# Optimization experiments

Measured on AMD Instinct MI355X. Metric: run time of the kernel, lower is better.

Reference implementation:

```python
import jax, jax.numpy as jnp
import numpy as np

B, T, D = 8, 2048, 256  # batch, time segments, feature dim (a_dim=v_dim=hidden=out=256)
EPS = 1e-8


def _layer_norm(x, g, b, eps=1e-6):
    m = jnp.mean(x, axis=-1, keepdims=True)
    v = jnp.var(x, axis=-1, keepdims=True)
    return (x - m) * jax.lax.rsqrt(v + eps) * g + b


def setup_inputs() -> dict:
    key = jax.random.key(0)
    ks = jax.random.split(key, 9)
    xav = lambda k: jax.random.uniform(k, (D, D), jnp.float32, -1.0, 1.0) * np.sqrt(6.0 / (D + D))
    return {
        "a_fea": jax.random.normal(ks[0], (B, T, D), jnp.float32),
        "v_fea": jax.random.normal(ks[1], (B, T, D), jnp.float32),
        "thr_val": jnp.float32(0.099),
        "Wv1": xav(ks[2]), "Wv2": xav(ks[3]), "Wvfc": xav(ks[4]),
        "Wa1": xav(ks[5]), "Wa2": xav(ks[6]), "Wafc": xav(ks[7]),
        "ln_g": jnp.ones((D,), jnp.float32),
        "ln_b": jnp.zeros((D,), jnp.float32),
    }


def reference(a_fea, v_fea, thr_val, Wv1, Wv2, Wvfc, Wa1, Wa2, Wafc, ln_g, ln_b):
    relu = jax.nn.relu
    # branch projections (dropout is identity at eval); torch Linear: x @ W.T
    v1 = relu(jnp.einsum('btd,hd->bth', v_fea, Wv1))
    v2 = relu(jnp.einsum('btd,hd->bth', v_fea, Wv2))
    a1 = relu(jnp.einsum('btd,hd->bth', a_fea, Wa1))
    a2 = relu(jnp.einsum('btd,hd->bth', a_fea, Wa2))

    d = v2.shape[-1]
    # scaled cross-modal scores, ReLU'd  [B, Tv, Ta]
    beta_va = relu(jnp.einsum('btd,bsd->bts', v2, a1) / jnp.sqrt(jnp.float32(d)))
    # a->v scores taken BEFORE row-normalization of beta_va (as in torch code)
    beta_av = jnp.transpose(beta_va, (0, 2, 1))

    time = beta_va.shape[-1]
    thr = thr_val * 10.0 / time

    # normalize -> threshold sparsify -> renormalize (v attends to a)
    bn_va = beta_va / (jnp.sum(beta_va, axis=-1, keepdims=True) + EPS)
    g_va = jnp.where(bn_va > thr, bn_va, 0.0)
    g_va = g_va / (jnp.sum(g_va, axis=-1, keepdims=True) + EPS)

    # same for a attends to v
    bn_av = beta_av / (jnp.sum(beta_av, axis=-1, keepdims=True) + EPS)
    g_av = jnp.where(bn_av > thr, bn_av, 0.0)
    g_av = g_av / (jnp.sum(g_av, axis=-1, keepdims=True) + EPS)

    # vectorized form of the diagonal selection double-loop (batch element 0)
    pred = (jnp.diagonal(g_av[0]) > 0).astype(jnp.float32)  # [T]

    a_pos = jnp.einsum('bts,bsd->btd', g_va, a2)
    v_psp = v_fea + a_pos
    v_pos = jnp.einsum('bts,bsd->btd', g_av, v1)
    a_psp = a_fea + v_pos

    v_psp = _layer_norm(relu(jnp.einsum('btd,od->bto', v_psp, Wvfc)), ln_g, ln_b)
    a_psp = _layer_norm(relu(jnp.einsum('btd,od->bto', a_psp, Wafc)), ln_g, ln_b)
    a_v_fuse = 0.5 * (v_psp + a_psp)
    return a_v_fuse, v_psp, a_psp, pred
```

## Files before the change

kernel.cpp:

```cpp
#include <hip/hip_runtime.h>
#include <math.h>

#define TT 2048
#define DD 256
#define NBATCH 8
#define EPSF 1e-8f

typedef unsigned short u16;
typedef __attribute__((ext_vector_type(8))) short short8;
typedef __attribute__((ext_vector_type(4))) float f32x4;

__device__ __forceinline__ u16 f2bf(float x) {
    unsigned int u = __builtin_bit_cast(unsigned int, x);
    u += 0x7fffu + ((u >> 16) & 1u);
    return (u16)(u >> 16);
}
__device__ __forceinline__ float bf2f(u16 h) {
    return __builtin_bit_cast(float, (unsigned int)h << 16);
}

__device__ __forceinline__ int frag_dst(int row, int k) {
    return (((row >> 4) * 4 + (k >> 3)) * 16 + (row & 15)) * 8 + (k & 7);
}

template<int BR>
__device__ __forceinline__ void stage_tile(const u16* __restrict__ g, u16* s,
                                           int row0, int k0, int ldk, int tid)
{
    #pragma unroll
    for (int i = 0; i < BR / 64; ++i) {
        const int c = tid + 256 * i;
        const int row = c >> 2, q = c & 3;
        *(int4*)(s + frag_dst(row, q * 8)) =
            *(const int4*)(g + (long)(row0 + row) * ldk + k0 + q * 8);
    }
}

__global__ __launch_bounds__(256)
void proj_kernel(const u16* __restrict__ vfh, const u16* __restrict__ vfl,
                 const u16* __restrict__ afh, const u16* __restrict__ afl,
                 const u16* __restrict__ Wsp,
                 u16* __restrict__ v2h, u16* __restrict__ v2l,
                 u16* __restrict__ a1h, u16* __restrict__ a1l,
                 u16* __restrict__ v1T, u16* __restrict__ a2T)
{
    const int zz = blockIdx.z;
    const u16* Ah = (zz == 1 || zz == 3) ? afh : vfh;
    const u16* Al = (zz == 1 || zz == 3) ? afl : vfl;
    const int widx = (zz == 0) ? 2 : (zz == 1) ? 4 : (zz == 2) ? 0 : 6;
    const u16* Bh = Wsp + widx * DD * DD;
    const u16* Bl = Bh + DD * DD;
    const bool split = zz < 2;
    u16* Oh = (zz == 0) ? v2h : a1h;
    u16* Ol = (zz == 0) ? v2l : a1l;
    u16* OT = (zz == 2) ? v1T : a2T;

    __shared__ __align__(16) u16 Ah_s[64 * 32], Al_s[64 * 32];
    __shared__ __align__(16) u16 Bh_s[64 * 32], Bl_s[64 * 32];
    const int m0 = blockIdx.y * 64, n0 = blockIdx.x * 64;
    const int tid = threadIdx.x, lane = tid & 63, w = tid >> 6;
    const int wy = w >> 1, wx = w & 1;
    f32x4 acc[2][2] = {};

    for (int k0 = 0; k0 < DD; k0 += 32) {
        stage_tile<64>(Ah, Ah_s, m0, k0, DD, tid);
        stage_tile<64>(Al, Al_s, m0, k0, DD, tid);
        stage_tile<64>(Bh, Bh_s, n0, k0, DD, tid);
        stage_tile<64>(Bl, Bl_s, n0, k0, DD, tid);
        __syncthreads();
        short8 ah[2], al[2], bh[2], bl[2];
        #pragma unroll
        for (int i = 0; i < 2; ++i) {
            ah[i] = *(const short8*)(Ah_s + ((wy * 2 + i) * 64 + lane) * 8);
            al[i] = *(const short8*)(Al_s + ((wy * 2 + i) * 64 + lane) * 8);
        }
        #pragma unroll
        for (int j = 0; j < 2; ++j) {
            bh[j] = *(const short8*)(Bh_s + ((wx * 2 + j) * 64 + lane) * 8);
            bl[j] = *(const short8*)(Bl_s + ((wx * 2 + j) * 64 + lane) * 8);
        }
        #pragma unroll
        for (int i = 0; i < 2; ++i)
            #pragma unroll
            for (int j = 0; j < 2; ++j) {
                acc[i][j] = __builtin_amdgcn_mfma_f32_16x16x32_bf16(ah[i], bl[j], acc[i][j], 0, 0, 0);
                acc[i][j] = __builtin_amdgcn_mfma_f32_16x16x32_bf16(al[i], bh[j], acc[i][j], 0, 0, 0);
                acc[i][j] = __builtin_amdgcn_mfma_f32_16x16x32_bf16(ah[i], bh[j], acc[i][j], 0, 0, 0);
            }
        __syncthreads();
    }
    const int quad = lane >> 4, col = lane & 15;
    #pragma unroll
    for (int i = 0; i < 2; ++i)
        #pragma unroll
        for (int j = 0; j < 2; ++j) {
            const int c = n0 + (wx * 2 + j) * 16 + col;
            const int rbase = m0 + (wy * 2 + i) * 16 + quad * 4;
            if (split) {
                #pragma unroll
                for (int r = 0; r < 4; ++r) {
                    const float v = fmaxf(acc[i][j][r], 0.f);
                    const u16 h = f2bf(v);
                    Oh[(long)(rbase + r) * DD + c] = h;
                    Ol[(long)(rbase + r) * DD + c] = f2bf(v - bf2f(h));
                }
            } else {
                short4 pk;
                pk.x = (short)f2bf(fmaxf(acc[i][j][0], 0.f));
                pk.y = (short)f2bf(fmaxf(acc[i][j][1], 0.f));
                pk.z = (short)f2bf(fmaxf(acc[i][j][2], 0.f));
                pk.w = (short)f2bf(fmaxf(acc[i][j][3], 0.f));
                const int b = rbase >> 11, t = rbase & (TT - 1);
                *(short4*)(OT + ((long)b * DD + c) * TT + t) = pk;
            }
        }
}

__global__ __launch_bounds__(256)
void score_kernel(const u16* __restrict__ v2h, const u16* __restrict__ v2l,
                  const u16* __restrict__ a1h, const u16* __restrict__ a1l,
                  u16* __restrict__ beta, u16* __restrict__ betaT,
                  float* __restrict__ rs, float* __restrict__ cs)
{
    __shared__ __align__(16) u16 Ah_s[128 * 32], Al_s[128 * 32];
    __shared__ __align__(16) u16 Bh_s[128 * 32], Bl_s[128 * 32];
    const int z = blockIdx.z;
    const int m0 = blockIdx.y * 128, n0 = blockIdx.x * 128;
    const int tid = threadIdx.x, lane = tid & 63, w = tid >> 6;
    const int wy = w >> 1, wx = w & 1;
    const long zoff = (long)z * TT * DD;
    f32x4 acc[4][4] = {};

    for (int k0 = 0; k0 < DD; k0 += 32) {
        stage_tile<128>(v2h + zoff, Ah_s, m0, k0, DD, tid);
        stage_tile<128>(v2l + zoff, Al_s, m0, k0, DD, tid);
        stage_tile<128>(a1h + zoff, Bh_s, n0, k0, DD, tid);
        stage_tile<128>(a1l + zoff, Bl_s, n0, k0, DD, tid);
        __syncthreads();
        short8 ah[4], al[4], bh[4], bl[4];
        #pragma unroll
        for (int i = 0; i < 4; ++i) {
            ah[i] = *(const short8*)(Ah_s + ((wy * 4 + i) * 64 + lane) * 8);
            al[i] = *(const short8*)(Al_s + ((wy * 4 + i) * 64 + lane) * 8);
        }
        #pragma unroll
        for (int j = 0; j < 4; ++j) {
            bh[j] = *(const short8*)(Bh_s + ((wx * 4 + j) * 64 + lane) * 8);
            bl[j] = *(const short8*)(Bl_s + ((wx * 4 + j) * 64 + lane) * 8);
        }
        #pragma unroll
        for (int i = 0; i < 4; ++i)
            #pragma unroll
            for (int j = 0; j < 4; ++j) {
                acc[i][j] = __builtin_amdgcn_mfma_f32_16x16x32_bf16(ah[i], bl[j], acc[i][j], 0, 0, 0);
                acc[i][j] = __builtin_amdgcn_mfma_f32_16x16x32_bf16(al[i], bh[j], acc[i][j], 0, 0, 0);
                acc[i][j] = __builtin_amdgcn_mfma_f32_16x16x32_bf16(ah[i], bh[j], acc[i][j], 0, 0, 0);
            }
        __syncthreads();
    }

    const int quad = lane >> 4, col = lane & 15;
    const float scale = 1.f / 16.f;
    #pragma unroll
    for (int i = 0; i < 4; ++i)
        #pragma unroll
        for (int j = 0; j < 4; ++j) {
            const int c = n0 + (wx * 4 + j) * 16 + col;
            const int rbase = m0 + (wy * 4 + i) * 16 + quad * 4;
            short4 pk;
            #pragma unroll
            for (int r = 0; r < 4; ++r) {
                float v = fmaxf(acc[i][j][r] * scale, 0.f);
                acc[i][j][r] = v;
                const u16 h = f2bf(v);
                ((u16*)&pk)[r] = h;
                beta[((long)z * TT + rbase + r) * TT + c] = h;
            }
            *(short4*)(betaT + ((long)z * TT + c) * TT + rbase) = pk;
        }
    #pragma unroll
    for (int i = 0; i < 4; ++i)
        #pragma unroll
        for (int r = 0; r < 4; ++r) {
            float rp = 0.f;
            #pragma unroll
            for (int j = 0; j < 4; ++j) rp += acc[i][j][r];
            rp += __shfl_xor(rp, 1); rp += __shfl_xor(rp, 2);
            rp += __shfl_xor(rp, 4); rp += __shfl_xor(rp, 8);
            if (col == 0) {
                const int row = m0 + (wy * 4 + i) * 16 + quad * 4 + r;
                atomicAdd(&rs[(long)z * TT + row], rp);
            }
        }
    #pragma unroll
    for (int j = 0; j < 4; ++j) {
        float cp = 0.f;
        #pragma unroll
        for (int i = 0; i < 4; ++i)
            #pragma unroll
            for (int r = 0; r < 4; ++r) cp += acc[i][j][r];
        cp += __shfl_xor(cp, 16); cp += __shfl_xor(cp, 32);
        if (lane < 16) {
            const int c = n0 + (wx * 4 + j) * 16 + col;
            atomicAdd(&cs[(long)z * TT + c], cp);
        }
    }
}

__global__ __launch_bounds__(256)
void pv_kernel(const u16* __restrict__ beta, const u16* __restrict__ betaT,
               const u16* __restrict__ a2T, const u16* __restrict__ v1T,
               const float* __restrict__ rs, const float* __restrict__ cs,
               const float* __restrict__ thrp,
               const float* __restrict__ v_fea, const float* __restrict__ a_fea,
               u16* __restrict__ yvin, u16* __restrict__ yain)
{
    __shared__ __align__(16) u16 A_s[128 * 32], B_s[64 * 32];
    __shared__ float sthr[128], sA[128], ssum[128];
    const int zz = blockIdx.z;
    const int z = zz & 7;
    const bool av = zz >= 8;
    const u16* P      = av ? betaT : beta;
    const u16* VT     = av ? v1T : a2T;
    const float* sums = av ? cs : rs;
    const float* resid = av ? a_fea : v_fea;
    u16* outb         = av ? yain : yvin;

    const int m0 = blockIdx.y * 128, n0 = blockIdx.x * 64;
    const int tid = threadIdx.x, lane = tid & 63, w = tid >> 6;
    const int wy = w >> 1, wx = w & 1;
    const float thr = thrp[0] * 10.0f / (float)TT;
    if (tid < 128) {
        const float s = sums[(long)z * TT + m0 + tid];
        sA[tid] = s; sthr[tid] = thr * (s + EPSF); ssum[tid] = 0.f;
    }
    __syncthreads();
    f32x4 acc[4][2] = {};
    float rpart[2] = {0.f, 0.f};
    const int arow = tid >> 2, aq = tid & 3;

    for (int k0 = 0; k0 < TT; k0 += 32) {
        #pragma unroll
        for (int i = 0; i < 2; ++i) {
            const int row = arow + 64 * i;
            union { int4 v; u16 us[8]; } U;
            U.v = *(const int4*)(P + ((long)z * TT + m0 + row) * TT + k0 + aq * 8);
            const float ct = sthr[row];
            float ss = 0.f;
            #pragma unroll
            for (int t = 0; t < 8; ++t) {
                const float v = bf2f(U.us[t]);
                if (v > ct) ss += v; else U.us[t] = 0;
            }
            *(int4*)(A_s + frag_dst(row, aq * 8)) = U.v;
            rpart[i] += ss;
        }
        stage_tile<64>(VT + (long)z * DD * TT, B_s, n0, k0, TT, tid);
        __syncthreads();
        short8 a[4], b[2];
        #pragma unroll
        for (int i = 0; i < 4; ++i)
            a[i] = *(const short8*)(A_s + ((wy * 4 + i) * 64 + lane) * 8);
        #pragma unroll
        for (int j = 0; j < 2; ++j)
            b[j] = *(const short8*)(B_s + ((wx * 2 + j) * 64 + lane) * 8);
        #pragma unroll
        for (int i = 0; i < 4; ++i)
            #pragma unroll
            for (int j = 0; j < 2; ++j)
                acc[i][j] = __builtin_amdgcn_mfma_f32_16x16x32_bf16(a[i], b[j], acc[i][j], 0, 0, 0);
        __syncthreads();
    }
    atomicAdd(&ssum[arow], rpart[0]);
    atomicAdd(&ssum[arow + 64], rpart[1]);
    __syncthreads();

    const int quad = lane >> 4, col = lane & 15;
    #pragma unroll
    for (int i = 0; i < 4; ++i)
        #pragma unroll
        for (int j = 0; j < 2; ++j) {
            const int c = n0 + (wx * 2 + j) * 16 + col;
            #pragma unroll
            for (int r = 0; r < 4; ++r) {
                const int lrow = (wy * 4 + i) * 16 + quad * 4 + r;
                const int row = m0 + lrow;
                const float inv = 1.0f / (ssum[lrow] + EPSF * (sA[lrow] + EPSF));
                const float v = acc[i][j][r] * inv + resid[((long)z * TT + row) * DD + c];
                outb[((long)z * TT + row) * DD + c] = f2bf(v);
            }
        }
}

__global__ __launch_bounds__(256)
void fc_kernel(const u16* __restrict__ Ain, const u16* __restrict__ Wb,
               float* __restrict__ Cf)
{
    const int z = blockIdx.z;
    const u16* A = Ain + (size_t)z * (size_t)NBATCH * TT * DD;
    const u16* B = Wb + (size_t)z * DD * DD;
    float* C = Cf + (size_t)z * (size_t)NBATCH * TT * DD;
    __shared__ __align__(16) u16 A_s[128 * 32], B_s[64 * 32];
    const int m0 = blockIdx.y * 128, n0 = blockIdx.x * 64;
    const int tid = threadIdx.x, lane = tid & 63, w = tid >> 6;
    const int wy = w >> 1, wx = w & 1;
    f32x4 acc[4][2] = {};
    for (int k0 = 0; k0 < DD; k0 += 32) {
        stage_tile<128>(A, A_s, m0, k0, DD, tid);
        stage_tile<64>(B, B_s, n0, k0, DD, tid);
        __syncthreads();
        short8 a[4], b[2];
        #pragma unroll
        for (int i = 0; i < 4; ++i)
            a[i] = *(const short8*)(A_s + ((wy * 4 + i) * 64 + lane) * 8);
        #pragma unroll
        for (int j = 0; j < 2; ++j)
            b[j] = *(const short8*)(B_s + ((wx * 2 + j) * 64 + lane) * 8);
        #pragma unroll
        for (int i = 0; i < 4; ++i)
            #pragma unroll
            for (int j = 0; j < 2; ++j)
                acc[i][j] = __builtin_amdgcn_mfma_f32_16x16x32_bf16(a[i], b[j], acc[i][j], 0, 0, 0);
        __syncthreads();
    }
    const int quad = lane >> 4, col = lane & 15;
    #pragma unroll
    for (int i = 0; i < 4; ++i)
        #pragma unroll
        for (int j = 0; j < 2; ++j) {
            const int c = n0 + (wx * 2 + j) * 16 + col;
            #pragma unroll
            for (int r = 0; r < 4; ++r) {
                const int row = m0 + (wy * 4 + i) * 16 + quad * 4 + r;
                C[(long)row * DD + c] = fmaxf(acc[i][j][r], 0.f);
            }
        }
}

__global__ __launch_bounds__(256)
void pred_exact(const float* __restrict__ vf, const float* __restrict__ af,
                const float* __restrict__ Wv2, const float* __restrict__ Wa1,
                const float* __restrict__ cs, const float* __restrict__ thrp,
                float* __restrict__ pred)
{
    __shared__ float vs[8][260];
    __shared__ float as_[8][260];
    __shared__ float red[4][8];
    const int t0 = blockIdx.x * 8;
    const int tid = threadIdx.x;
    {
        const int i = tid >> 5, c = (tid & 31) * 8;
        *(float4*)&vs[i][c] = *(const float4*)(vf + (long)(t0 + i) * DD + c);
        *(float4*)&vs[i][c + 4] = *(const float4*)(vf + (long)(t0 + i) * DD + c + 4);
        *(float4*)&as_[i][c] = *(const float4*)(af + (long)(t0 + i) * DD + c);
        *(float4*)&as_[i][c + 4] = *(const float4*)(af + (long)(t0 + i) * DD + c + 4);
    }
    __syncthreads();
    const int j = tid;
    float av[8] = {0.f}, aa[8] = {0.f};
    for (int k = 0; k < DD; k += 4) {
        const float4 wv = *(const float4*)(Wv2 + (long)j * DD + k);
        const float4 wa = *(const float4*)(Wa1 + (long)j * DD + k);
        #pragma unroll
        for (int i = 0; i < 8; ++i) {
            const float4 x = *(const float4*)&vs[i][k];
            av[i] += wv.x * x.x + wv.y * x.y + wv.z * x.z + wv.w * x.w;
            const float4 y = *(const float4*)&as_[i][k];
            aa[i] += wa.x * y.x + wa.y * y.y + wa.z * y.z + wa.w * y.w;
        }
    }
    float p[8];
    #pragma unroll
    for (int i = 0; i < 8; ++i)
        p[i] = fmaxf(av[i], 0.f) * fmaxf(aa[i], 0.f);
    #pragma unroll
    for (int off = 32; off > 0; off >>= 1)
        #pragma unroll
        for (int i = 0; i < 8; ++i) p[i] += __shfl_xor(p[i], off);
    const int lane = tid & 63, wv_ = tid >> 6;
    if (lane == 0)
        #pragma unroll
        for (int i = 0; i < 8; ++i) red[wv_][i] = p[i];
    __syncthreads();
    if (tid < 8) {
        float d = red[0][tid] + red[1][tid] + red[2][tid] + red[3][tid];
        d = fmaxf(d * (1.f / 16.f), 0.f);
        const float thr = thrp[0] * 10.0f / (float)TT;
        pred[t0 + tid] = (d > thr * (cs[t0 + tid] + EPSF)) ? 1.0f : 0.0f;
    }
}

__global__ __launch_bounds__(256)
void split_feat(const float* __restrict__ vf, const float* __restrict__ af,
                u16* __restrict__ vfh, u16* __restrict__ vfl,
                u16* __restrict__ afh, u16* __restrict__ afl)
{
    const long i4 = ((long)blockIdx.x * 256 + threadIdx.x) * 4;
    const float* src = blockIdx.y ? af : vf;
    u16* dh = blockIdx.y ? afh : vfh;
    u16* dl = blockIdx.y ? afl : vfl;
    float4 a = *(const float4*)(src + i4);
    ushort4 h4, l4; u16 h;
    h = f2bf(a.x); h4.x = h; l4.x = f2bf(a.x - bf2f(h));
    h = f2bf(a.y); h4.y = h; l4.y = f2bf(a.y - bf2f(h));
    h = f2bf(a.z); h4.z = h; l4.z = f2bf(a.z - bf2f(h));
    h = f2bf(a.w); h4.w = h; l4.w = f2bf(a.w - bf2f(h));
    *(ushort4*)(dh + i4) = h4;
    *(ushort4*)(dl + i4) = l4;
}

__global__ __launch_bounds__(256)
void split_w(const float* __restrict__ w0, const float* __restrict__ w1,
             const float* __restrict__ w2, const float* __restrict__ w3,
             const float* __restrict__ w4, const float* __restrict__ w5,
             u16* __restrict__ out)
{
    const int t = blockIdx.y;
    const float* w = (t == 0) ? w0 : (t == 1) ? w1 : (t == 2) ? w2
                   : (t == 3) ? w3 : (t == 4) ? w4 : w5;
    const int i4 = (blockIdx.x * 256 + threadIdx.x) * 4;
    float4 a = *(const float4*)(w + i4);
    if (t < 4) {
        u16* oh = out + (size_t)t * 2 * DD * DD;
        u16* ol = oh + DD * DD;
        ushort4 h4, l4; u16 h;
        h = f2bf(a.x); h4.x = h; l4.x = f2bf(a.x - bf2f(h));
        h = f2bf(a.y); h4.y = h; l4.y = f2bf(a.y - bf2f(h));
        h = f2bf(a.z); h4.z = h; l4.z = f2bf(a.z - bf2f(h));
        h = f2bf(a.w); h4.w = h; l4.w = f2bf(a.w - bf2f(h));
        *(ushort4*)(oh + i4) = h4;
        *(ushort4*)(ol + i4) = l4;
    } else {
        u16* ob = out + (size_t)8 * DD * DD + (size_t)(t - 4) * DD * DD;
        ushort4 o;
        o.x = f2bf(a.x); o.y = f2bf(a.y); o.z = f2bf(a.z); o.w = f2bf(a.w);
        *(ushort4*)(ob + i4) = o;
    }
}

__global__ __launch_bounds__(256)
void ln_fuse_kernel(const float* __restrict__ yv, const float* __restrict__ ya,
                    const float* __restrict__ g, const float* __restrict__ b,
                    float* __restrict__ fuse, float* __restrict__ vpsp,
                    float* __restrict__ apsp)
{
    const long row = (long)blockIdx.x * 4 + (threadIdx.x >> 6);
    const int lane = threadIdx.x & 63;
    const float4 xv = *(const float4*)(yv + row * DD + lane * 4);
    const float4 xa = *(const float4*)(ya + row * DD + lane * 4);
    float sv = xv.x + xv.y + xv.z + xv.w;
    float sa = xa.x + xa.y + xa.z + xa.w;
    #pragma unroll
    for (int off = 32; off > 0; off >>= 1) {
        sv += __shfl_xor(sv, off);
        sa += __shfl_xor(sa, off);
    }
    const float mv = sv * (1.f / 256.f);
    const float ma = sa * (1.f / 256.f);
    const float dv0 = xv.x - mv, dv1 = xv.y - mv, dv2 = xv.z - mv, dv3 = xv.w - mv;
    const float da0 = xa.x - ma, da1 = xa.y - ma, da2 = xa.z - ma, da3 = xa.w - ma;
    float qv = dv0 * dv0 + dv1 * dv1 + dv2 * dv2 + dv3 * dv3;
    float qa = da0 * da0 + da1 * da1 + da2 * da2 + da3 * da3;
    #pragma unroll
    for (int off = 32; off > 0; off >>= 1) {
        qv += __shfl_xor(qv, off);
        qa += __shfl_xor(qa, off);
    }
    const float rv = rsqrtf(qv * (1.f / 256.f) + 1e-6f);
    const float ra = rsqrtf(qa * (1.f / 256.f) + 1e-6f);
    const float4 gg = *(const float4*)(g + lane * 4);
    const float4 bb = *(const float4*)(b + lane * 4);
    float4 ov, oa, of;
    ov.x = dv0 * rv * gg.x + bb.x; ov.y = dv1 * rv * gg.y + bb.y;
    ov.z = dv2 * rv * gg.z + bb.z; ov.w = dv3 * rv * gg.w + bb.w;
    oa.x = da0 * ra * gg.x + bb.x; oa.y = da1 * ra * gg.y + bb.y;
    oa.z = da2 * ra * gg.z + bb.z; oa.w = da3 * ra * gg.w + bb.w;
    of.x = 0.5f * (ov.x + oa.x); of.y = 0.5f * (ov.y + oa.y);
    of.z = 0.5f * (ov.z + oa.z); of.w = 0.5f * (ov.w + oa.w);
    *(float4*)(vpsp + row * DD + lane * 4) = ov;
    *(float4*)(apsp + row * DD + lane * 4) = oa;
    *(float4*)(fuse + row * DD + lane * 4) = of;
}

extern "C" void kernel_launch(void* const* d_in, const int* in_sizes, int n_in,
                              void* d_out, int out_size, void* d_ws, size_t ws_size,
                              hipStream_t stream)
{
    const float* a_fea = (const float*)d_in[0];
    const float* v_fea = (const float*)d_in[1];
    const float* thrp  = (const float*)d_in[2];
    const float* Wv1   = (const float*)d_in[3];
    const float* Wv2   = (const float*)d_in[4];
    const float* Wvfc  = (const float*)d_in[5];
    const float* Wa1   = (const float*)d_in[6];
    const float* Wa2   = (const float*)d_in[7];
    const float* Wafc  = (const float*)d_in[8];
    const float* lng   = (const float*)d_in[9];
    const float* lnb   = (const float*)d_in[10];

    const long MT = (long)NBATCH * TT;
    float* out_fuse = (float*)d_out;
    float* out_vpsp = out_fuse + MT * DD;
    float* out_apsp = out_vpsp + MT * DD;
    float* out_pred = out_apsp + MT * DD;

    char* ws = (char*)d_ws;
    const size_t fb = (size_t)MT * DD * sizeof(u16);
    const size_t sumB = (size_t)MT * sizeof(float);
    u16* v2h  = (u16*)(ws + 0 * fb);
    u16* v2l  = (u16*)(ws + 1 * fb);
    u16* a1h  = (u16*)(ws + 2 * fb);
    u16* a1l  = (u16*)(ws + 3 * fb);
    u16* yvin = (u16*)(ws + 4 * fb);
    u16* yain = (u16*)(ws + 5 * fb);
    u16* v1T  = (u16*)(ws + 6 * fb);
    u16* a2T  = (u16*)(ws + 7 * fb);
    char* p = ws + 8 * fb;
    float* rs = (float*)(p + 0 * sumB);
    float* cs = (float*)(p + 1 * sumB);
    u16* Wsp  = (u16*)(p + 2 * sumB);
    char* q = p + 2 * sumB + 10 * DD * DD * sizeof(u16);
    const size_t betaB = (size_t)NBATCH * TT * TT * sizeof(u16);
    u16* beta  = (u16*)q;
    u16* betaT = (u16*)(q + betaB);
    u16* vfh = (u16*)q;
    u16* vfl = vfh + MT * DD;
    u16* afh = vfl + MT * DD;
    u16* afl = afh + MT * DD;
    float* yv = (float*)(ws + 0 * fb);
    float* ya = (float*)(ws + 2 * fb);

    hipMemsetAsync(rs, 0, 2 * sumB, stream);

    const dim3 blk(256, 1, 1);

    split_feat<<<dim3((unsigned)(MT * DD / 1024), 2, 1), blk, 0, stream>>>(
        v_fea, a_fea, vfh, vfl, afh, afl);
    split_w<<<dim3(DD * DD / 1024, 6, 1), blk, 0, stream>>>(
        Wv1, Wv2, Wa1, Wa2, Wvfc, Wafc, Wsp);

    proj_kernel<<<dim3(DD / 64, (unsigned)(MT / 64), 4), blk, 0, stream>>>(
        vfh, vfl, afh, afl, Wsp, v2h, v2l, a1h, a1l, v1T, a2T);

    score_kernel<<<dim3(TT / 128, TT / 128, NBATCH), blk, 0, stream>>>(
        v2h, v2l, a1h, a1l, beta, betaT, rs, cs);
    pred_exact<<<dim3(TT / 8, 1, 1), blk, 0, stream>>>(
        v_fea, a_fea, Wv2, Wa1, cs, thrp, out_pred);

    pv_kernel<<<dim3(DD / 64, TT / 128, 2 * NBATCH), blk, 0, stream>>>(
        beta, betaT, a2T, v1T, rs, cs, thrp, v_fea, a_fea, yvin, yain);

    fc_kernel<<<dim3(DD / 64, (unsigned)(MT / 128), 2), blk, 0, stream>>>(
        yvin, Wsp + 8 * DD * DD, yv);
    ln_fuse_kernel<<<dim3((unsigned)(MT / 4), 1, 1), blk, 0, stream>>>(
        yv, ya, lng, lnb, out_fuse, out_vpsp, out_apsp);
}
```

Before: 446.4 us.

## Stage betaT transpose through LDS and widen pv_kernel to full output width

score_kernel now writes the transposed score matrix by staging the bf16 tile in padded shared memory and emitting coalesced 16-byte row stores, replacing the strided short4 column writes. pv_kernel is restructured so each 512-thread block covers all 256 output columns for 128 rows. The thresholded probability row is therefore read and filtered once instead of four times across column blocks. It also adds register prefetch of the next K-slice of P and V to overlap global loads with MFMA work. The costs are higher LDS use in score_kernel, extra syncs, and fewer, larger pv blocks (256 total), which may reduce occupancy.

```diff
diff --git a/kernel.cpp b/kernel.cpp
--- a/kernel.cpp
+++ b/kernel.cpp
@@ -122,8 +122,11 @@
                   u16* __restrict__ beta, u16* __restrict__ betaT,
                   float* __restrict__ rs, float* __restrict__ cs)
 {
-    __shared__ __align__(16) u16 Ah_s[128 * 32], Al_s[128 * 32];
-    __shared__ __align__(16) u16 Bh_s[128 * 32], Bl_s[128 * 32];
+    __shared__ __align__(16) u16 S[128 * 136];
+    u16* Ah_s = S;
+    u16* Al_s = S + 4096;
+    u16* Bh_s = S + 8192;
+    u16* Bl_s = S + 12288;
     const int z = blockIdx.z;
     const int m0 = blockIdx.y * 128, n0 = blockIdx.x * 128;
     const int tid = threadIdx.x, lane = tid & 63, w = tid >> 6;
@@ -167,16 +170,12 @@
         for (int j = 0; j < 4; ++j) {
             const int c = n0 + (wx * 4 + j) * 16 + col;
             const int rbase = m0 + (wy * 4 + i) * 16 + quad * 4;
-            short4 pk;
             #pragma unroll
             for (int r = 0; r < 4; ++r) {
                 float v = fmaxf(acc[i][j][r] * scale, 0.f);
                 acc[i][j][r] = v;
-                const u16 h = f2bf(v);
-                ((u16*)&pk)[r] = h;
-                beta[((long)z * TT + rbase + r) * TT + c] = h;
-            }
-            *(short4*)(betaT + ((long)z * TT + c) * TT + rbase) = pk;
+                beta[((long)z * TT + rbase + r) * TT + c] = f2bf(v);
+            }
         }
     #pragma unroll
     for (int i = 0; i < 4; ++i)
@@ -205,9 +204,31 @@
             atomicAdd(&cs[(long)z * TT + c], cp);
         }
     }
-}
-
-__global__ __launch_bounds__(256)
+    __syncthreads();
+    #pragma unroll
+    for (int i = 0; i < 4; ++i)
+        #pragma unroll
+        for (int j = 0; j < 4; ++j) {
+            const int cl = (wx * 4 + j) * 16 + col;
+            const int rl = (wy * 4 + i) * 16 + quad * 4;
+            short4 pk;
+            pk.x = (short)f2bf(acc[i][j][0]);
+            pk.y = (short)f2bf(acc[i][j][1]);
+            pk.z = (short)f2bf(acc[i][j][2]);
+            pk.w = (short)f2bf(acc[i][j][3]);
+            *(short4*)(S + cl * 136 + rl) = pk;
+        }
+    __syncthreads();
+    #pragma unroll
+    for (int it = 0; it < 8; ++it) {
+        const int idx = tid + 256 * it;
+        const int cl = idx >> 4, tq = idx & 15;
+        const int4 v = *(const int4*)(S + cl * 136 + tq * 8);
+        *(int4*)(betaT + ((long)z * TT + n0 + cl) * TT + m0 + tq * 8) = v;
+    }
+}
+
+__global__ __launch_bounds__(512)
 void pv_kernel(const u16* __restrict__ beta, const u16* __restrict__ betaT,
                const u16* __restrict__ a2T, const u16* __restrict__ v1T,
                const float* __restrict__ rs, const float* __restrict__ cs,
@@ -215,9 +236,10 @@
                const float* __restrict__ v_fea, const float* __restrict__ a_fea,
                u16* __restrict__ yvin, u16* __restrict__ yain)
 {
-    __shared__ __align__(16) u16 A_s[128 * 32], B_s[64 * 32];
+    __shared__ __align__(16) u16 A_s[128 * 32], B_s[256 * 32];
     __shared__ float sthr[128], sA[128], ssum[128];
-    const int zz = blockIdx.z;
+    const int zz = blockIdx.x;
+    const int m0 = blockIdx.y * 128;
     const int z = zz & 7;
     const bool av = zz >= 8;
     const u16* P      = av ? betaT : beta;
@@ -226,61 +248,67 @@
     const float* resid = av ? a_fea : v_fea;
     u16* outb         = av ? yain : yvin;
 
-    const int m0 = blockIdx.y * 128, n0 = blockIdx.x * 64;
     const int tid = threadIdx.x, lane = tid & 63, w = tid >> 6;
-    const int wy = w >> 1, wx = w & 1;
+    const int wy = w >> 2, wx = w & 3;
     const float thr = thrp[0] * 10.0f / (float)TT;
     if (tid < 128) {
         const float s = sums[(long)z * TT + m0 + tid];
         sA[tid] = s; sthr[tid] = thr * (s + EPSF); ssum[tid] = 0.f;
     }
     __syncthreads();
-    f32x4 acc[4][2] = {};
-    float rpart[2] = {0.f, 0.f};
+    f32x4 acc[4][4] = {};
+    float rpart = 0.f;
     const int arow = tid >> 2, aq = tid & 3;
+    const u16* Pp = P + ((long)z * TT + m0 + arow) * TT + aq * 8;
+    const u16* V0 = VT + (long)z * DD * TT + (long)arow * TT + aq * 8;
+    const u16* V1 = V0 + (long)128 * TT;
+
+    int4 Ar  = *(const int4*)(Pp);
+    int4 Br0 = *(const int4*)(V0);
+    int4 Br1 = *(const int4*)(V1);
 
     for (int k0 = 0; k0 < TT; k0 += 32) {
-        #pragma unroll
-        for (int i = 0; i < 2; ++i) {
-            const int row = arow + 64 * i;
-            union { int4 v; u16 us[8]; } U;
-            U.v = *(const int4*)(P + ((long)z * TT + m0 + row) * TT + k0 + aq * 8);
-            const float ct = sthr[row];
-            float ss = 0.f;
-            #pragma unroll
-            for (int t = 0; t < 8; ++t) {
-                const float v = bf2f(U.us[t]);
-                if (v > ct) ss += v; else U.us[t] = 0;
-            }
-            *(int4*)(A_s + frag_dst(row, aq * 8)) = U.v;
-            rpart[i] += ss;
-        }
-        stage_tile<64>(VT + (long)z * DD * TT, B_s, n0, k0, TT, tid);
-        __syncthreads();
-        short8 a[4], b[2];
+        union { int4 v; u16 us[8]; } U;
+        U.v = Ar;
+        const float ct = sthr[arow];
+        float ss = 0.f;
+        #pragma unroll
+        for (int t = 0; t < 8; ++t) {
+            const float v = bf2f(U.us[t]);
+            if (v > ct) ss += v; else U.us[t] = 0;
+        }
+        rpart += ss;
+        *(int4*)(A_s + frag_dst(arow, aq * 8)) = U.v;
+        *(int4*)(B_s + frag_dst(arow, aq * 8)) = Br0;
+        *(int4*)(B_s + frag_dst(arow + 128, aq * 8)) = Br1;
+        __syncthreads();
+        const int kn = (k0 + 32 < TT) ? (k0 + 32) : k0;
+        Ar  = *(const int4*)(Pp + kn);
+        Br0 = *(const int4*)(V0 + kn);
+        Br1 = *(const int4*)(V1 + kn);
+        short8 a[4], b[4];
         #pragma unroll
         for (int i = 0; i < 4; ++i)
             a[i] = *(const short8*)(A_s + ((wy * 4 + i) * 64 + lane) * 8);
         #pragma unroll
-        for (int j = 0; j < 2; ++j)
-            b[j] = *(const short8*)(B_s + ((wx * 2 + j) * 64 + lane) * 8);
+        for (int j = 0; j < 4; ++j)
+            b[j] = *(const short8*)(B_s + ((wx * 4 + j) * 64 + lane) * 8);
         #pragma unroll
         for (int i = 0; i < 4; ++i)
             #pragma unroll
-            for (int j = 0; j < 2; ++j)
+            for (int j = 0; j < 4; ++j)
                 acc[i][j] = __builtin_amdgcn_mfma_f32_16x16x32_bf16(a[i], b[j], acc[i][j], 0, 0, 0);
         __syncthreads();
     }
-    atomicAdd(&ssum[arow], rpart[0]);
-    atomicAdd(&ssum[arow + 64], rpart[1]);
+    atomicAdd(&ssum[arow], rpart);
     __syncthreads();
 
     const int quad = lane >> 4, col = lane & 15;
     #pragma unroll
     for (int i = 0; i < 4; ++i)
         #pragma unroll
-        for (int j = 0; j < 2; ++j) {
-            const int c = n0 + (wx * 2 + j) * 16 + col;
+        for (int j = 0; j < 4; ++j) {
+            const int c = (wx * 4 + j) * 16 + col;
             #pragma unroll
             for (int r = 0; r < 4; ++r) {
                 const int lrow = (wy * 4 + i) * 16 + quad * 4 + r;
@@ -547,7 +575,7 @@
     pred_exact<<<dim3(TT / 8, 1, 1), blk, 0, stream>>>(
         v_fea, a_fea, Wv2, Wa1, cs, thrp, out_pred);
 
-    pv_kernel<<<dim3(DD / 64, TT / 128, 2 * NBATCH), blk, 0, stream>>>(
+    pv_kernel<<<dim3(2 * NBATCH, TT / 128, 1), dim3(512, 1, 1), 0, stream>>>(
         beta, betaT, a2T, v1T, rs, cs, thrp, v_fea, a_fea, yvin, yain);
 
     fc_kernel<<<dim3(DD / 64, (unsigned)(MT / 128), 2), blk, 0, stream>>>(
```

Measured after the change: 445.1 us. About the same (-0.3%).
